# Optimization experiments

Measured on AMD Instinct MI355X. Metric: run time of the kernel, lower is better.

The kernel has to match this reference:

```python
import jax, jax.numpy as jnp
import numpy as np

B = 65536
D = 512
D_ID = 256   # identity features (mask <= 0): indices 0..255
D_TR = 256   # transform features (mask > 0): indices 256..511
H = 1024     # hidden_features


def setup_inputs() -> dict:
    key = jax.random.key(0)
    ks = jax.random.split(key, 9)
    s = lambda fan_in: 1.0 / np.sqrt(fan_in)
    return {
        "x":  jax.random.normal(ks[0], (B, D), dtype=jnp.float32),
        # weights stored [in, out] (jax convention; torch Linear uses x @ W.T)
        "W1": jax.random.uniform(ks[1], (D_ID, H), minval=-s(D_ID), maxval=s(D_ID), dtype=jnp.float32),
        "b1": jax.random.uniform(ks[2], (H,), minval=-s(D_ID), maxval=s(D_ID), dtype=jnp.float32),
        "W2": jax.random.uniform(ks[3], (H, H), minval=-s(H), maxval=s(H), dtype=jnp.float32),
        "b2": jax.random.uniform(ks[4], (H,), minval=-s(H), maxval=s(H), dtype=jnp.float32),
        "W3": jax.random.uniform(ks[5], (H, H), minval=-s(H), maxval=s(H), dtype=jnp.float32),
        "b3": jax.random.uniform(ks[6], (H,), minval=-s(H), maxval=s(H), dtype=jnp.float32),
        "W4": jax.random.uniform(ks[7], (H, 2 * D_TR), minval=-s(H), maxval=s(H), dtype=jnp.float32),
        "b4": jax.random.uniform(ks[8], (2 * D_TR,), minval=-s(H), maxval=s(H), dtype=jnp.float32),
    }


def reference(x, W1, b1, W2, b2, W3, b3, W4, b4):
    # contiguous half/half mask: identity = first 256 feats, transform = last 256
    identity_split = x[:, :D_ID]            # [B, D_ID]
    transform_split = x[:, D_ID:]           # [B, D_TR]

    # transform_net: Linear+ReLU x3, then Linear to 2*D_TR
    h = jax.nn.relu(identity_split @ W1 + b1)
    h = jax.nn.relu(h @ W2 + b2)
    h = jax.nn.relu(h @ W3 + b3)
    params = h @ W4 + b4                     # [B, 2*D_TR]

    shift = params[:, :D_TR]
    unconstrained_scale = params[:, D_TR:]
    scale = jax.nn.sigmoid(unconstrained_scale + 2.0) + 0.001
    log_scale = jnp.log(scale)

    transformed = transform_split * scale + shift
    outputs = jnp.concatenate([identity_split, transformed], axis=1)  # scatter back
    logabsdet = jnp.sum(log_scale, axis=1)   # sum_except_batch
    return outputs, logabsdet
```

## Files before the change

### kernel.cpp

```cpp
#include <hip/hip_runtime.h>
#include <hip/hip_bf16.h>
#include <cstdint>
#include <cstddef>

typedef __attribute__((ext_vector_type(4))) int   i32x4;
typedef __attribute__((ext_vector_type(4))) float f32x4;

#define DEVI static __device__ __forceinline__

DEVI void gload_lds16(const void* g, void* l) {
    __builtin_amdgcn_global_load_lds((const __attribute__((address_space(1))) void*)g,
                                     (__attribute__((address_space(3))) void*)l, 16, 0, 0);
}

#define BARR() __builtin_amdgcn_s_barrier()
#define LGKM0() do { asm volatile("s_waitcnt lgkmcnt(0)" ::: "memory"); \
                     __builtin_amdgcn_sched_barrier(0); } while (0)
#define SCHED0() __builtin_amdgcn_sched_barrier(0)
#define VMW(n) asm volatile("s_waitcnt vmcnt(" #n ")" ::: "memory")
#define SP(x) __builtin_amdgcn_s_setprio(x)

DEVI int q8(float v, float s) {
    int q = __float2int_rn(v * s);
    return q < -127 ? -127 : (q > 127 ? 127 : q);
}

__global__ __launch_bounds__(256)
void prep_x_kernel(const float* __restrict__ x, char* __restrict__ xq,
                   float* __restrict__ out) {
    int g = blockIdx.x * 256 + threadIdx.x;
    int row = g >> 5, c8 = (g & 31) * 8;
    const float4 v0 = *(const float4*)(x + (size_t)row * 512 + c8);
    const float4 v1 = *(const float4*)(x + (size_t)row * 512 + c8 + 4);
    *(float4*)(out + (size_t)row * 512 + c8)     = v0;
    *(float4*)(out + (size_t)row * 512 + c8 + 4) = v1;
    unsigned p0 = (q8(v0.x,20.f)&255) | ((q8(v0.y,20.f)&255)<<8) |
                  ((q8(v0.z,20.f)&255)<<16) | ((unsigned)(q8(v0.w,20.f)&255)<<24);
    unsigned p1 = (q8(v1.x,20.f)&255) | ((q8(v1.y,20.f)&255)<<8) |
                  ((q8(v1.z,20.f)&255)<<16) | ((unsigned)(q8(v1.w,20.f)&255)<<24);
    *(int2*)(xq + (size_t)row * 256 + c8) = make_int2((int)p0, (int)p1);
}

__global__ __launch_bounds__(256)
void prep_w_kernel(const float* __restrict__ W1, const float* __restrict__ W2,
                   const float* __restrict__ W3, const float* __restrict__ W4,
                   const float* __restrict__ b4, char* __restrict__ W1q,
                   char* __restrict__ W2q, char* __restrict__ W3q,
                   char* __restrict__ W4q, float* __restrict__ b4p) {
    int idx = blockIdx.x * 256 + threadIdx.x;
    if (idx < 262144) {
        int n = idx >> 8, k = idx & 255;
        W1q[idx] = (char)q8(W1[(size_t)k * 1024 + n], 2032.f);
    } else if (idx < 262144 + 1048576) {
        int j = idx - 262144;
        int n = j >> 10, k = j & 1023;
        W2q[j] = (char)q8(W2[(size_t)k * 1024 + n], 4064.f);
    } else if (idx < 262144 + 2097152) {
        int j = idx - 262144 - 1048576;
        int n = j >> 10, k = j & 1023;
        W3q[j] = (char)q8(W3[(size_t)k * 1024 + n], 4064.f);
    } else {
        int j = idx - 262144 - 2097152;
        int vt = j >> 10, k = j & 1023;
        int bn = vt >> 8, v = vt & 255;
        int v16 = v >> 4, c = v & 15;
        int tcol = bn * 128 + (v16 >> 1) * 16 + c;
        int col = (v16 & 1) ? 256 + tcol : tcol;
        W4q[j] = (char)q8(W4[(size_t)k * 512 + col], 4064.f);
        if (k == 0) b4p[vt] = b4[col];
    }
}

#define RD_A(DST, g) do { \
    const char* _b = lds + ((g) & 3) * 32768; \
    _Pragma("unroll") \
    for (int m = 0; m < 8; ++m) DST[m] = *(const i32x4*)(_b + aOff + m * 1024); \
} while (0)

#define RD_B(DST, g, J0) do { \
    const char* _b = lds + ((g) & 3) * 32768 + 16384; \
    DST[0] = *(const i32x4*)(_b + bOff + (J0) * 1024); \
    DST[1] = *(const i32x4*)(_b + bOff + (J0 + 1) * 1024); \
} while (0)

#define MM2(BSET, ASET, J0) do { \
    _Pragma("unroll") \
    for (int m = 0; m < 8; ++m) { \
        acc[m][J0]     = __builtin_amdgcn_mfma_i32_16x16x64_i8(BSET[0], ASET[m], acc[m][J0], 0, 0, 0); \
        acc[m][J0 + 1] = __builtin_amdgcn_mfma_i32_16x16x64_i8(BSET[1], ASET[m], acc[m][J0 + 1], 0, 0, 0); \
    } \
} while (0)

#define PHASE0(ASET, t) do { \
    RD_B(b1, (t), 2); \
    STAGE_A((t) + 3); \
    SCHED0(); \
    SP(1); MM2(b0, ASET, 0); SP(0); \
    LGKM0(); BARR(); \
} while (0)

#define PHASE1(ASET, ANXT, t, W0) do { \
    if (W0) { VMW(0); } else { VMW(6); } \
    RD_A(ANXT, (t) + 1); \
    RD_B(b0, (t) + 1, 0); \
    STAGE_B((t) + 3); \
    SCHED0(); \
    SP(1); MM2(b1, ASET, 2); SP(0); \
    LGKM0(); BARR(); \
} while (0)

template<int MODE, int NI, int TPB>
__global__ __launch_bounds__(512)
void gemmR_kernel(const char* __restrict__ A, const char* __restrict__ Bt,
                  const float* __restrict__ bias, void* __restrict__ Cp,
                  const float* __restrict__ x, float* __restrict__ part,
                  int N, int K, int gx, float invS) {
    constexpr int GT = NI * TPB;
    __shared__ __align__(16) char lds[131072];

    const int tid = threadIdx.x;
    const int bid = blockIdx.x;
    const int xcd = bid & 7, bidx = bid >> 3;
    const int bn = bidx % gx;
    const int mgrp = bidx / gx;
    const int colBase = bn * 256;
    const int l  = tid & 63;
    const int w  = tid >> 6;
    const int wm = w >> 2, wn = w & 3;
    const int lr = l & 15, lq = l >> 4;
    const int qa = lq ^ ((lr >> 1) & 3);

    const int aOff = (wm * 128 + lr) * 64 + qa * 16;
    const int bOff = (wn * 64 + lr) * 64 + qa * 16;

    const int sar = tid >> 2;
    const int ca = (((tid & 3) ^ ((tid >> 3) & 3))) * 16;

    auto rowBaseOf = [&](int tt) { return (xcd * 32 + mgrp * TPB + tt) * 256; };

    auto STAGE_A = [&](int gd) {
        const int gs = gd < GT ? gd : GT - 1;
        char* dst = lds + (gd & 3) * 32768 + tid * 16;
        const char* src = A + (size_t)(rowBaseOf(gs / NI) + sar) * K
                            + (gs & (NI - 1)) * 64 + ca;
#pragma unroll
        for (int u = 0; u < 2; ++u)
            gload_lds16(src + (size_t)u * 128 * K, dst + u * 8192);
    };
    auto STAGE_B = [&](int gd) {
        const int gs = gd < GT ? gd : GT - 1;
        char* dst = lds + (gd & 3) * 32768 + 16384 + tid * 16;
        const char* src = Bt + (size_t)(colBase + sar) * K
                             + (gs & (NI - 1)) * 64 + ca;
#pragma unroll
        for (int u = 0; u < 2; ++u)
            gload_lds16(src + (size_t)u * 128 * K, dst + u * 8192);
    };

    i32x4 acc[8][4];
    const i32x4 zero = {0, 0, 0, 0};
#pragma unroll
    for (int m = 0; m < 8; ++m)
#pragma unroll
        for (int n = 0; n < 4; ++n) acc[m][n] = zero;
    i32x4 afX[8], afY[8], b0[2], b1[2];

    auto epi = [&](int tt) {
        float4 bv[4];
#pragma unroll
        for (int n = 0; n < 4; ++n)
            bv[n] = *(const float4*)(bias + colBase + wn * 64 + n * 16 + lq * 4);
        const int rowBase = rowBaseOf(tt);
        const int row0 = rowBase + wm * 128;
        if (MODE == 0) {
            char* C = (char*)Cp;
#pragma unroll
            for (int m = 0; m < 8; ++m) {
                const int row = row0 + m * 16 + lr;
#pragma unroll
                for (int n = 0; n < 4; ++n) {
                    unsigned pack = 0;
#pragma unroll
                    for (int r = 0; r < 4; ++r) {
                        float v = (float)acc[m][n][r] * invS + ((const float*)&bv[n])[r];
                        v = fmaxf(v, 0.f);
                        int q = (int)(fminf(v, 7.9f) * 16.f + 0.5f);
                        pack |= (unsigned)q << (8 * r);
                    }
                    *(int*)(C + (size_t)row * N + colBase + wn * 64 + n * 16 + lq * 4) = (int)pack;
                }
            }
        } else {
            const int B = 65536;
            float* out = (float*)Cp;
#pragma unroll
            for (int m = 0; m < 8; ++m) {
                const int row = row0 + m * 16 + lr;
                float lsum = 0.f;
#pragma unroll
                for (int p = 0; p < 2; ++p) {
                    const int tcol = bn * 128 + wn * 32 + p * 16 + lq * 4;
                    const float4 xt = *(const float4*)(x + (size_t)row * 512 + 256 + tcol);
                    float4 ov;
#pragma unroll
                    for (int r = 0; r < 4; ++r) {
                        float sh = (float)acc[m][2 * p][r]     * invS + ((const float*)&bv[2 * p])[r];
                        float u  = (float)acc[m][2 * p + 1][r] * invS + ((const float*)&bv[2 * p + 1])[r];
                        float s  = 1.f / (1.f + __expf(-(u + 2.f))) + 0.001f;
                        ((float*)&ov)[r] = ((const float*)&xt)[r] * s + sh;
                        lsum += __logf(s);
                    }
                    *(float4*)(out + (size_t)row * 512 + 256 + tcol) = ov;
                }
                lsum += __shfl_xor(lsum, 16);
                lsum += __shfl_xor(lsum, 32);
                if (lq == 0) part[(size_t)(bn * 4 + wn) * B + row] = lsum;
            }
        }
#pragma unroll
        for (int m = 0; m < 8; ++m)
#pragma unroll
            for (int n = 0; n < 4; ++n) acc[m][n] = zero;
    };

    STAGE_A(0); STAGE_B(0); STAGE_A(1); STAGE_B(1); STAGE_A(2); STAGE_B(2);
    VMW(0);
    BARR();
    RD_A(afX, 0); RD_B(b0, 0, 0);
    LGKM0();

#pragma unroll 1
    for (int g = 0; g < GT / 2; ++g) {
        const int ta = 2 * g, tb = 2 * g + 1;
        const bool w0 = (ta > 0) && ((ta & (NI - 1)) == 0);
        PHASE0(afX, ta);
        PHASE1(afX, afY, ta, w0);
        PHASE0(afY, tb);
        PHASE1(afY, afX, tb, false);
        if (((tb + 1) & (NI - 1)) == 0) epi((tb + 1) / NI - 1);
    }
}

__global__ __launch_bounds__(256)
void lad_reduce_kernel(const float* __restrict__ part, float* __restrict__ lad) {
    const int B = 65536;
    int rIdx = blockIdx.x * 256 + threadIdx.x;
    float s = 0.f;
#pragma unroll
    for (int j = 0; j < 8; ++j) s += part[(size_t)j * B + rIdx];
    lad[rIdx] = s;
}

extern "C" void kernel_launch(void* const* d_in, const int* in_sizes, int n_in,
                              void* d_out, int out_size, void* d_ws, size_t ws_size,
                              hipStream_t stream) {
    const int B = 65536, D_ID = 256, H = 1024, NP = 512;

    const float* x  = (const float*)d_in[0];
    const float* W1 = (const float*)d_in[1];
    const float* b1 = (const float*)d_in[2];
    const float* W2 = (const float*)d_in[3];
    const float* b2 = (const float*)d_in[4];
    const float* W3 = (const float*)d_in[5];
    const float* b3 = (const float*)d_in[6];
    const float* W4 = (const float*)d_in[7];
    const float* b4 = (const float*)d_in[8];

    float* out = (float*)d_out;
    float* lad = out + (size_t)B * 512;

    const float invS1  = 1.f / (20.f * 2032.f);
    const float invS23 = 1.f / (16.f * 4064.f);

    char* ws = (char*)d_ws;
    const size_t hbytes = (size_t)B * H;
    char*  hA   = ws;
    char*  hB   = ws + hbytes;
    char*  xq   = ws + hbytes;
    float* part = (float*)(ws + hbytes);
    char*  W1q  = ws + 2 * hbytes;
    char*  W2q  = W1q + (size_t)H * D_ID;
    char*  W3q  = W2q + (size_t)H * H;
    char*  W4q  = W3q + (size_t)H * H;
    float* b4p  = (float*)(W4q + (size_t)NP * H);

    dim3 blk(256), blk8(512);
    prep_x_kernel<<<dim3(B * 32 / 256), blk, 0, stream>>>(x, xq, out);
    prep_w_kernel<<<dim3(11264), blk, 0, stream>>>(W1, W2, W3, W4, b4,
                                                   W1q, W2q, W3q, W4q, b4p);

    gemmR_kernel<0, 4, 4><<<dim3(256), blk8, 0, stream>>>(xq, W1q, b1, hA, nullptr, nullptr, H, D_ID, 4, invS1);
    gemmR_kernel<0, 16, 4><<<dim3(256), blk8, 0, stream>>>(hA, W2q, b2, hB, nullptr, nullptr, H, H, 4, invS23);
    gemmR_kernel<0, 16, 4><<<dim3(256), blk8, 0, stream>>>(hB, W3q, b3, hA, nullptr, nullptr, H, H, 4, invS23);
    gemmR_kernel<2, 16, 2><<<dim3(256), blk8, 0, stream>>>(hA, W4q, b4p, out, x, part, NP, H, 2, invS23);

    lad_reduce_kernel<<<dim3(B / 256), blk, 0, stream>>>(part, lad);
}
```

Baseline: 335.8 us.

## Add K=128 double-buffered int8 GEMM variant for first and last layers

Adds a new gemmQ kernel that stages 128-wide K tiles into two 64 KB LDS buffers with an 8-chunk XOR swizzle. It reads all A and B fragments for a tile at once and issues two half-tile MFMA batches, with the next tile's global-to-LDS load placed between them. This kernel replaces the four-stage 64-wide pipeline for layer 1 (K=256) and layer 4 (the fused output epilogue), cutting barrier and loop overhead per unit of work. The cost is only double buffering, so load latency is less hidden, and register pressure is higher from holding 16 A and 8 B fragments.

Result: faster. 325.6 us (-3.0%).

```diff
diff --git a/kernel.cpp b/kernel.cpp
--- a/kernel.cpp
+++ b/kernel.cpp
@@ -71,51 +71,36 @@
     }
 }
 
-#define RD_A(DST, g) do { \
-    const char* _b = lds + ((g) & 3) * 32768; \
-    _Pragma("unroll") \
-    for (int m = 0; m < 8; ++m) DST[m] = *(const i32x4*)(_b + aOff + m * 1024); \
-} while (0)
-
-#define RD_B(DST, g, J0) do { \
-    const char* _b = lds + ((g) & 3) * 32768 + 16384; \
-    DST[0] = *(const i32x4*)(_b + bOff + (J0) * 1024); \
-    DST[1] = *(const i32x4*)(_b + bOff + (J0 + 1) * 1024); \
-} while (0)
-
-#define MM2(BSET, ASET, J0) do { \
-    _Pragma("unroll") \
-    for (int m = 0; m < 8; ++m) { \
-        acc[m][J0]     = __builtin_amdgcn_mfma_i32_16x16x64_i8(BSET[0], ASET[m], acc[m][J0], 0, 0, 0); \
-        acc[m][J0 + 1] = __builtin_amdgcn_mfma_i32_16x16x64_i8(BSET[1], ASET[m], acc[m][J0 + 1], 0, 0, 0); \
-    } \
-} while (0)
-
-#define PHASE0(ASET, t) do { \
-    RD_B(b1, (t), 2); \
-    STAGE_A((t) + 3); \
-    SCHED0(); \
-    SP(1); MM2(b0, ASET, 0); SP(0); \
-    LGKM0(); BARR(); \
-} while (0)
-
-#define PHASE1(ASET, ANXT, t, W0) do { \
-    if (W0) { VMW(0); } else { VMW(6); } \
-    RD_A(ANXT, (t) + 1); \
-    RD_B(b0, (t) + 1, 0); \
-    STAGE_B((t) + 3); \
-    SCHED0(); \
-    SP(1); MM2(b1, ASET, 2); SP(0); \
-    LGKM0(); BARR(); \
-} while (0)
-
-template<int MODE, int NI, int TPB>
+#define QRDS(p) do { \
+    const char* _a = lds + (p) * 65536; \
+    const char* _bb = _a + 32768; \
+    _Pragma("unroll") \
+    for (int mt = 0; mt < 8; ++mt) aF[mt][0] = *(const i32x4*)(_a + aRow + mt * 2048 + ck0); \
+    _Pragma("unroll") \
+    for (int nt = 0; nt < 4; ++nt) bF[nt][0] = *(const i32x4*)(_bb + bRow + nt * 2048 + ck0); \
+    _Pragma("unroll") \
+    for (int mt = 0; mt < 8; ++mt) aF[mt][1] = *(const i32x4*)(_a + aRow + mt * 2048 + ck1); \
+    _Pragma("unroll") \
+    for (int nt = 0; nt < 4; ++nt) bF[nt][1] = *(const i32x4*)(_bb + bRow + nt * 2048 + ck1); \
+} while (0)
+
+#define QMMH(S) do { \
+    SP(1); \
+    _Pragma("unroll") \
+    for (int mt = 0; mt < 8; ++mt) \
+        _Pragma("unroll") \
+        for (int nt = 0; nt < 4; ++nt) \
+            acc[mt][nt] = __builtin_amdgcn_mfma_i32_16x16x64_i8(bF[nt][S], aF[mt][S], acc[mt][nt], 0, 0, 0); \
+    SP(0); \
+} while (0)
+
+template<int MODE, int NI2, int TPB>
 __global__ __launch_bounds__(512)
-void gemmR_kernel(const char* __restrict__ A, const char* __restrict__ Bt,
+void gemmQ_kernel(const char* __restrict__ A, const char* __restrict__ Bt,
                   const float* __restrict__ bias, void* __restrict__ Cp,
                   const float* __restrict__ x, float* __restrict__ part,
                   int N, int K, int gx, float invS) {
-    constexpr int GT = NI * TPB;
+    constexpr int GT = NI2 * TPB;
     __shared__ __align__(16) char lds[131072];
 
     const int tid = threadIdx.x;
@@ -128,33 +113,33 @@
     const int w  = tid >> 6;
     const int wm = w >> 2, wn = w & 3;
     const int lr = l & 15, lq = l >> 4;
-    const int qa = lq ^ ((lr >> 1) & 3);
-
-    const int aOff = (wm * 128 + lr) * 64 + qa * 16;
-    const int bOff = (wn * 64 + lr) * 64 + qa * 16;
-
-    const int sar = tid >> 2;
-    const int ca = (((tid & 3) ^ ((tid >> 3) & 3))) * 16;
+    const int gsw = (lr >> 1) & 7;
+
+    const int aRow = (wm * 128 + lr) * 128;
+    const int bRow = (wn * 64 + lr) * 128;
+    const int ck0 = ((lq ^ gsw) & 7) * 16;
+    const int ck1 = (((4 | lq) ^ gsw) & 7) * 16;
 
     auto rowBaseOf = [&](int tt) { return (xcd * 32 + mgrp * TPB + tt) * 256; };
 
-    auto STAGE_A = [&](int gd) {
+    auto STAGE = [&](int gd) {
         const int gs = gd < GT ? gd : GT - 1;
-        char* dst = lds + (gd & 3) * 32768 + tid * 16;
-        const char* src = A + (size_t)(rowBaseOf(gs / NI) + sar) * K
-                            + (gs & (NI - 1)) * 64 + ca;
-#pragma unroll
-        for (int u = 0; u < 2; ++u)
-            gload_lds16(src + (size_t)u * 128 * K, dst + u * 8192);
-    };
-    auto STAGE_B = [&](int gd) {
-        const int gs = gd < GT ? gd : GT - 1;
-        char* dst = lds + (gd & 3) * 32768 + 16384 + tid * 16;
-        const char* src = Bt + (size_t)(colBase + sar) * K
-                             + (gs & (NI - 1)) * 64 + ca;
-#pragma unroll
-        for (int u = 0; u < 2; ++u)
-            gload_lds16(src + (size_t)u * 128 * K, dst + u * 8192);
+        const int kb = (gs & (NI2 - 1)) * 128;
+        const int arb = rowBaseOf(gs / NI2);
+        char* da = lds + (gd & 1) * 65536;
+#pragma unroll
+        for (int u = 0; u < 4; ++u) {
+            int row = u * 64 + (tid >> 3);
+            int c = (tid & 7) ^ ((row >> 1) & 7);
+            gload_lds16(A + (size_t)(arb + row) * K + kb + c * 16, da + u * 8192 + tid * 16);
+        }
+        char* db = lds + (gd & 1) * 65536 + 32768;
+#pragma unroll
+        for (int u = 0; u < 4; ++u) {
+            int row = u * 64 + (tid >> 3);
+            int c = (tid & 7) ^ ((row >> 1) & 7);
+            gload_lds16(Bt + (size_t)(colBase + row) * K + kb + c * 16, db + u * 8192 + tid * 16);
+        }
     };
 
     i32x4 acc[8][4];
@@ -163,7 +148,7 @@
     for (int m = 0; m < 8; ++m)
 #pragma unroll
         for (int n = 0; n < 4; ++n) acc[m][n] = zero;
-    i32x4 afX[8], afY[8], b0[2], b1[2];
+    i32x4 aF[8][2], bF[4][2];
 
     auto epi = [&](int tt) {
         float4 bv[4];
@@ -223,6 +208,179 @@
             for (int n = 0; n < 4; ++n) acc[m][n] = zero;
     };
 
+    STAGE(0); STAGE(1);
+    VMW(0);
+    BARR();
+
+#pragma unroll 1
+    for (int t = 0; t < GT; ++t) {
+        const int p = t & 1;
+        QRDS(p);
+        QMMH(0);
+        LGKM0();
+        BARR();
+        SCHED0();
+        STAGE(t + 2);
+        QMMH(1);
+        VMW(8);
+        SCHED0();
+        BARR();
+        if (((t + 1) & (NI2 - 1)) == 0) epi((t + 1) / NI2 - 1);
+    }
+}
+
+#define RD_A(DST, g) do { \
+    const char* _b = lds + ((g) & 3) * 32768; \
+    _Pragma("unroll") \
+    for (int m = 0; m < 8; ++m) DST[m] = *(const i32x4*)(_b + aOff + m * 1024); \
+} while (0)
+
+#define RD_B(DST, g, J0) do { \
+    const char* _b = lds + ((g) & 3) * 32768 + 16384; \
+    DST[0] = *(const i32x4*)(_b + bOff + (J0) * 1024); \
+    DST[1] = *(const i32x4*)(_b + bOff + (J0 + 1) * 1024); \
+} while (0)
+
+#define MM2(BSET, ASET, J0) do { \
+    _Pragma("unroll") \
+    for (int m = 0; m < 8; ++m) { \
+        acc[m][J0]     = __builtin_amdgcn_mfma_i32_16x16x64_i8(BSET[0], ASET[m], acc[m][J0], 0, 0, 0); \
+        acc[m][J0 + 1] = __builtin_amdgcn_mfma_i32_16x16x64_i8(BSET[1], ASET[m], acc[m][J0 + 1], 0, 0, 0); \
+    } \
+} while (0)
+
+#define PHASE0(ASET, t) do { \
+    RD_B(b1, (t), 2); \
+    STAGE_A((t) + 3); \
+    SCHED0(); \
+    SP(1); MM2(b0, ASET, 0); SP(0); \
+    LGKM0(); BARR(); \
+} while (0)
+
+#define PHASE1(ASET, ANXT, t, W0) do { \
+    if (W0) { VMW(0); } else { VMW(6); } \
+    RD_A(ANXT, (t) + 1); \
+    RD_B(b0, (t) + 1, 0); \
+    STAGE_B((t) + 3); \
+    SCHED0(); \
+    SP(1); MM2(b1, ASET, 2); SP(0); \
+    LGKM0(); BARR(); \
+} while (0)
+
+template<int MODE, int NI, int TPB>
+__global__ __launch_bounds__(512)
+void gemmR_kernel(const char* __restrict__ A, const char* __restrict__ Bt,
+                  const float* __restrict__ bias, void* __restrict__ Cp,
+                  const float* __restrict__ x, float* __restrict__ part,
+                  int N, int K, int gx, float invS) {
+    constexpr int GT = NI * TPB;
+    __shared__ __align__(16) char lds[131072];
+
+    const int tid = threadIdx.x;
+    const int bid = blockIdx.x;
+    const int xcd = bid & 7, bidx = bid >> 3;
+    const int bn = bidx % gx;
+    const int mgrp = bidx / gx;
+    const int colBase = bn * 256;
+    const int l  = tid & 63;
+    const int w  = tid >> 6;
+    const int wm = w >> 2, wn = w & 3;
+    const int lr = l & 15, lq = l >> 4;
+    const int qa = lq ^ ((lr >> 1) & 3);
+
+    const int aOff = (wm * 128 + lr) * 64 + qa * 16;
+    const int bOff = (wn * 64 + lr) * 64 + qa * 16;
+
+    const int sar = tid >> 2;
+    const int ca = (((tid & 3) ^ ((tid >> 3) & 3))) * 16;
+
+    auto rowBaseOf = [&](int tt) { return (xcd * 32 + mgrp * TPB + tt) * 256; };
+
+    auto STAGE_A = [&](int gd) {
+        const int gs = gd < GT ? gd : GT - 1;
+        char* dst = lds + (gd & 3) * 32768 + tid * 16;
+        const char* src = A + (size_t)(rowBaseOf(gs / NI) + sar) * K
+                            + (gs & (NI - 1)) * 64 + ca;
+#pragma unroll
+        for (int u = 0; u < 2; ++u)
+            gload_lds16(src + (size_t)u * 128 * K, dst + u * 8192);
+    };
+    auto STAGE_B = [&](int gd) {
+        const int gs = gd < GT ? gd : GT - 1;
+        char* dst = lds + (gd & 3) * 32768 + 16384 + tid * 16;
+        const char* src = Bt + (size_t)(colBase + sar) * K
+                             + (gs & (NI - 1)) * 64 + ca;
+#pragma unroll
+        for (int u = 0; u < 2; ++u)
+            gload_lds16(src + (size_t)u * 128 * K, dst + u * 8192);
+    };
+
+    i32x4 acc[8][4];
+    const i32x4 zero = {0, 0, 0, 0};
+#pragma unroll
+    for (int m = 0; m < 8; ++m)
+#pragma unroll
+        for (int n = 0; n < 4; ++n) acc[m][n] = zero;
+    i32x4 afX[8], afY[8], b0[2], b1[2];
+
+    auto epi = [&](int tt) {
+        float4 bv[4];
+#pragma unroll
+        for (int n = 0; n < 4; ++n)
+            bv[n] = *(const float4*)(bias + colBase + wn * 64 + n * 16 + lq * 4);
+        const int rowBase = rowBaseOf(tt);
+        const int row0 = rowBase + wm * 128;
+        if (MODE == 0) {
+            char* C = (char*)Cp;
+#pragma unroll
+            for (int m = 0; m < 8; ++m) {
+                const int row = row0 + m * 16 + lr;
+#pragma unroll
+                for (int n = 0; n < 4; ++n) {
+                    unsigned pack = 0;
+#pragma unroll
+                    for (int r = 0; r < 4; ++r) {
+                        float v = (float)acc[m][n][r] * invS + ((const float*)&bv[n])[r];
+                        v = fmaxf(v, 0.f);
+                        int q = (int)(fminf(v, 7.9f) * 16.f + 0.5f);
+                        pack |= (unsigned)q << (8 * r);
+                    }
+                    *(int*)(C + (size_t)row * N + colBase + wn * 64 + n * 16 + lq * 4) = (int)pack;
+                }
+            }
+        } else {
+            const int B = 65536;
+            float* out = (float*)Cp;
+#pragma unroll
+            for (int m = 0; m < 8; ++m) {
+                const int row = row0 + m * 16 + lr;
+                float lsum = 0.f;
+#pragma unroll
+                for (int p = 0; p < 2; ++p) {
+                    const int tcol = bn * 128 + wn * 32 + p * 16 + lq * 4;
+                    const float4 xt = *(const float4*)(x + (size_t)row * 512 + 256 + tcol);
+                    float4 ov;
+#pragma unroll
+                    for (int r = 0; r < 4; ++r) {
+                        float sh = (float)acc[m][2 * p][r]     * invS + ((const float*)&bv[2 * p])[r];
+                        float u  = (float)acc[m][2 * p + 1][r] * invS + ((const float*)&bv[2 * p + 1])[r];
+                        float s  = 1.f / (1.f + __expf(-(u + 2.f))) + 0.001f;
+                        ((float*)&ov)[r] = ((const float*)&xt)[r] * s + sh;
+                        lsum += __logf(s);
+                    }
+                    *(float4*)(out + (size_t)row * 512 + 256 + tcol) = ov;
+                }
+                lsum += __shfl_xor(lsum, 16);
+                lsum += __shfl_xor(lsum, 32);
+                if (lq == 0) part[(size_t)(bn * 4 + wn) * B + row] = lsum;
+            }
+        }
+#pragma unroll
+        for (int m = 0; m < 8; ++m)
+#pragma unroll
+            for (int n = 0; n < 4; ++n) acc[m][n] = zero;
+    };
+
     STAGE_A(0); STAGE_B(0); STAGE_A(1); STAGE_B(1); STAGE_A(2); STAGE_B(2);
     VMW(0);
     BARR();
@@ -289,10 +447,10 @@
     prep_w_kernel<<<dim3(11264), blk, 0, stream>>>(W1, W2, W3, W4, b4,
                                                    W1q, W2q, W3q, W4q, b4p);
 
-    gemmR_kernel<0, 4, 4><<<dim3(256), blk8, 0, stream>>>(xq, W1q, b1, hA, nullptr, nullptr, H, D_ID, 4, invS1);
+    gemmQ_kernel<0, 2, 4><<<dim3(256), blk8, 0, stream>>>(xq, W1q, b1, hA, nullptr, nullptr, H, D_ID, 4, invS1);
     gemmR_kernel<0, 16, 4><<<dim3(256), blk8, 0, stream>>>(hA, W2q, b2, hB, nullptr, nullptr, H, H, 4, invS23);
     gemmR_kernel<0, 16, 4><<<dim3(256), blk8, 0, stream>>>(hB, W3q, b3, hA, nullptr, nullptr, H, H, 4, invS23);
-    gemmR_kernel<2, 16, 2><<<dim3(256), blk8, 0, stream>>>(hA, W4q, b4p, out, x, part, NP, H, 2, invS23);
+    gemmQ_kernel<2, 8, 2><<<dim3(256), blk8, 0, stream>>>(hA, W4q, b4p, out, x, part, NP, H, 2, invS23);
 
     lad_reduce_kernel<<<dim3(B / 256), blk, 0, stream>>>(part, lad);
 }
```
